# Optimization experiments

Measured on AMD Instinct MI355X. Metric: run time of the kernel, lower is better.

Reference implementation:

```python
import jax, jax.numpy as jnp
import numpy as np

B, N, D_IN, D_OUT = 2, 2048, 2048, 2048
H, G = 16, 4            # num_heads, n_kv_groups
HD = D_OUT // H         # head_dim = 128
REP = H // G            # query heads per kv head = 4


def setup_inputs() -> dict:
    key = jax.random.key(0)
    ks = jax.random.split(key, 6)
    s = lambda fan_in: 1.0 / np.sqrt(fan_in)
    return {
        "x": jax.random.normal(ks[0], (B, N, D_IN), jnp.float32),
        "Wq": jax.random.normal(ks[1], (D_IN, D_OUT), jnp.float32) * s(D_IN),
        "Wk": jax.random.normal(ks[2], (D_IN, G * HD), jnp.float32) * s(D_IN),
        "Wv": jax.random.normal(ks[3], (D_IN, G * HD), jnp.float32) * s(D_IN),
        "Wo": jax.random.normal(ks[4], (D_OUT, D_OUT), jnp.float32) * s(D_OUT),
        "bo": jnp.zeros((D_OUT,), jnp.float32),
    }


def reference(x, Wq, Wk, Wv, Wo, bo):
    b, n, _ = x.shape
    # projections
    q = (x @ Wq).reshape(b, n, G, REP, HD)   # query heads grouped: h = g*REP + r
    k = (x @ Wk).reshape(b, n, G, HD)
    v = (x @ Wv).reshape(b, n, G, HD)
    # grouped attention scores; KV broadcast over REP instead of repeat_kv
    scores = jnp.einsum('bqgrd,bkgd->bgrqk', q, k)  # [b,G,REP,N,N]
    causal = jnp.tril(jnp.ones((n, n), bool))       # allowed positions
    scores = jnp.where(causal, scores, -jnp.inf)
    w = jax.nn.softmax(scores / np.float32(np.sqrt(HD)), axis=-1)
    ctx = jnp.einsum('bgrqk,bkgd->bqgrd', w, v).reshape(b, n, D_OUT)
    return ctx @ Wo + bo
```

## Files before the change

kernel.cpp:

```cpp
#include <hip/hip_runtime.h>
#include <stdint.h>

typedef __attribute__((ext_vector_type(8))) __bf16 bf16x8;
typedef __attribute__((ext_vector_type(4))) float f32x4;
typedef __attribute__((ext_vector_type(16))) float f32x16;
typedef __attribute__((ext_vector_type(4))) short short4v;
typedef __attribute__((ext_vector_type(4))) unsigned uint4v;

static constexpr int SEQ  = 2048;
static constexpr int DQKV = 3072;
static constexpr int HD   = 128;

__device__ __forceinline__ short f2bf(float f) {
  unsigned u = __builtin_bit_cast(unsigned, f);
  u += 0x7fffu + ((u >> 16) & 1u);
  return (short)(u >> 16);
}

__device__ __forceinline__ unsigned pack2(float a, float b) {
  return (unsigned)(unsigned short)f2bf(a) | ((unsigned)(unsigned short)f2bf(b) << 16);
}

__device__ __forceinline__ void gl_lds16(const void* g, void* l) {
  __builtin_amdgcn_global_load_lds(
      (const __attribute__((address_space(1))) void*)g,
      (__attribute__((address_space(3))) void*)l, 16, 0, 0);
}

__global__ __launch_bounds__(256)
void prep_kernel(const float* __restrict__ x, const float* __restrict__ Wq,
                 const float* __restrict__ Wk, const float* __restrict__ Wv,
                 const float* __restrict__ Wo,
                 short* __restrict__ xb, short* __restrict__ WqkvT,
                 short* __restrict__ WoT) {
  int blk = blockIdx.x, tid = threadIdx.x;
  if (blk < 8192) {
    int i = blk * 256 + tid;
    float4 v = reinterpret_cast<const float4*>(x)[i];
    short4v o;
    o[0] = f2bf(v.x); o[1] = f2bf(v.y); o[2] = f2bf(v.z); o[3] = f2bf(v.w);
    *reinterpret_cast<short4v*>(xb + (size_t)i * 4) = o;
    return;
  }
  blk -= 8192;
  __shared__ float tile[32][33];
  const float* in; short* out; int C, bx, by;
  if (blk < 4096)      { in = Wq; out = WqkvT;                     C = 2048; bx = blk & 63; by = blk >> 6; }
  else if (blk < 5120) { int t = blk - 4096; in = Wk; out = WqkvT + (size_t)2048 * 2048; C = 512; bx = t & 15; by = t >> 4; }
  else if (blk < 6144) { int t = blk - 5120; in = Wv; out = WqkvT + (size_t)2560 * 2048; C = 512; bx = t & 15; by = t >> 4; }
  else                 { int t = blk - 6144; in = Wo; out = WoT;   C = 2048; bx = t & 63; by = t >> 6; }
  const int R = 2048;
  int c0 = bx * 32, r0 = by * 32, tx = tid & 31, ty = tid >> 5;
  for (int i = 0; i < 4; i++)
    tile[ty + i * 8][tx] = in[(size_t)(r0 + ty + i * 8) * C + c0 + tx];
  __syncthreads();
  for (int i = 0; i < 4; i++)
    out[(size_t)(c0 + ty + i * 8) * R + r0 + tx] = f2bf(tile[tx][ty + i * 8]);
}

__global__ __launch_bounds__(256) void transpose_v_kernel(const short* __restrict__ qkv,
                                                          short* __restrict__ vT) {
  __shared__ short tile[32][33];
  int n0 = blockIdx.x * 32, c0 = blockIdx.y * 32, b = blockIdx.z;
  int tx = threadIdx.x & 31, ty = threadIdx.x >> 5;
  for (int i = 0; i < 4; i++)
    tile[ty + i * 8][tx] = qkv[(size_t)(b * SEQ + n0 + ty + i * 8) * DQKV + 2560 + c0 + tx];
  __syncthreads();
  for (int i = 0; i < 4; i++)
    vT[(size_t)(b * 512 + c0 + ty + i * 8) * SEQ + n0 + tx] = tile[tx][ty + i * 8];
}

template <int F32OUT>
__global__ __launch_bounds__(256)
void gemm_bt_kernel(const short* __restrict__ A, const short* __restrict__ BT,
                    void* __restrict__ Cout, const float* __restrict__ bias,
                    int M, int N, int K, int qcols, float qscale) {
  __shared__ __align__(16) short As[8192];
  __shared__ __align__(16) short Bs[8192];
  const int tid = threadIdx.x, lane = tid & 63, w = tid >> 6;
  const int l15 = lane & 15, quad = lane >> 4, q8 = quad * 8;
  const int row0 = blockIdx.y * 128, col0 = blockIdx.x * 128;
  const int wm = (w >> 1) * 64, wn = (w & 1) * 64;
  f32x4 acc[4][4] = {};
  const short* ga0 = A  + (size_t)(row0 + w * 16 + (lane >> 2)) * K + (lane & 3) * 8;
  const short* gb0 = BT + (size_t)(col0 + w * 16 + (lane >> 2)) * K + (lane & 3) * 8;
  for (int kt = 0; kt < K; kt += 64) {
    for (int s = 0; s < 2; s++) {
      gl_lds16(ga0 + kt + s * 32,                  As + s * 4096 + w * 512);
      gl_lds16(ga0 + (size_t)64 * K + kt + s * 32, As + s * 4096 + 2048 + w * 512);
      gl_lds16(gb0 + kt + s * 32,                  Bs + s * 4096 + w * 512);
      gl_lds16(gb0 + (size_t)64 * K + kt + s * 32, Bs + s * 4096 + 2048 + w * 512);
    }
    __syncthreads();
    for (int s = 0; s < 2; s++) {
      bf16x8 af[4], bfr[4];
      for (int i = 0; i < 4; i++)
        af[i] = *reinterpret_cast<const bf16x8*>(As + s * 4096 + (wm + i * 16 + l15) * 32 + q8);
      for (int j = 0; j < 4; j++)
        bfr[j] = *reinterpret_cast<const bf16x8*>(Bs + s * 4096 + (wn + j * 16 + l15) * 32 + q8);
      for (int i = 0; i < 4; i++)
        for (int j = 0; j < 4; j++)
          acc[i][j] = __builtin_amdgcn_mfma_f32_16x16x32_bf16(af[i], bfr[j], acc[i][j], 0, 0, 0);
    }
    __syncthreads();
  }
  if (F32OUT) {
    float* C = (float*)Cout;
    for (int j = 0; j < 4; j++) {
      int col = col0 + wn + j * 16 + l15;
      float bv = bias[col];
      for (int i = 0; i < 4; i++)
        for (int r = 0; r < 4; r++)
          C[(size_t)(row0 + wm + i * 16 + quad * 4 + r) * N + col] = acc[i][j][r] + bv;
    }
  } else {
    short* C = (short*)Cout;
    for (int j = 0; j < 4; j++) {
      int col = col0 + wn + j * 16 + l15;
      float sc = (col < qcols) ? qscale : 1.0f;
      for (int i = 0; i < 4; i++)
        for (int r = 0; r < 4; r++)
          C[(size_t)(row0 + wm + i * 16 + quad * 4 + r) * N + col] = f2bf(acc[i][j][r] * sc);
    }
  }
}

__global__ __launch_bounds__(256, 2)
void attn_kernel(const short* __restrict__ qkv, const short* __restrict__ vT,
                 short* __restrict__ ctx) {
  __shared__ __align__(16) short Ks[2 * 8192];
  __shared__ __align__(16) float Oex[2 * 4096];
  __shared__ float lbuf[4 * 32];
  const int tid = threadIdx.x, lane = tid & 63, w = tid >> 6;
  const int l31 = lane & 31, hi = lane >> 5;
  const int qh = w & 1, kh = w >> 1;
  const int idx = blockIdx.x;
  const int p = idx >> 5, h = (idx >> 1) & 15, b = idx & 1, g = h >> 2;
  const int qtA = 31 - p, qtB = p;
  const int lenA = qtA + 1, total = lenA + qtB + 1;

  auto stageK = [&](int buf, int kt) {
    const short* gk = qkv + (size_t)(b * SEQ + kt * 64) * DQKV + 2048 + g * HD;
#pragma unroll
    for (int s = 0; s < 4; s++) {
      const int r = w * 16 + s * 4 + (lane >> 4);
      gl_lds16(gk + (size_t)r * DQKV + ((lane & 15) ^ (r & 7)) * 8,
               Ks + buf * 8192 + (w * 16 + s * 4) * 128);
    }
  };

  bf16x8 qf[8];
  f32x16 o_acc[4] = {};
  float lsum = 0.f;

  stageK(0, 0);
  for (int t = 0; t < total; t++) {
    const int seg = (t >= lenA);
    const int kt = seg ? (t - lenA) : t;
    const int qt = seg ? qtB : qtA;
    const int cur = t & 1;
    __syncthreads();

    if (t == 0 || t == lenA) {
      const short* gq = qkv + (size_t)(b * SEQ + qt * 64 + qh * 32 + l31) * DQKV + h * HD + hi * 8;
#pragma unroll
      for (int d = 0; d < 8; d++) qf[d] = *reinterpret_cast<const bf16x8*>(gq + d * 16);
    }

    bf16x8 vf[4][2];
#pragma unroll
    for (int dt = 0; dt < 4; dt++)
#pragma unroll
      for (int sub = 0; sub < 2; sub++)
        vf[dt][sub] = *reinterpret_cast<const bf16x8*>(
            vT + (size_t)(b * 512 + g * HD + dt * 32 + l31) * SEQ +
            kt * 64 + (kh * 2 + sub) * 16 + hi * 8);
    __builtin_amdgcn_sched_barrier(0);

    if (t + 1 < total) {
      const int nkt = (t + 1 >= lenA) ? (t + 1 - lenA) : (t + 1);
      stageK(cur ^ 1, nkt);
    }
    __builtin_amdgcn_sched_barrier(0);

    const short* Kb = Ks + cur * 8192;
    f32x16 sa0 = {}, sa1 = {};
    __builtin_amdgcn_s_setprio(1);
#pragma unroll
    for (int d = 0; d < 4; d++) {
      bf16x8 kf0 = *reinterpret_cast<const bf16x8*>(
          Kb + (kh * 32 + l31) * 128 + (((2 * d + hi) ^ (l31 & 7)) * 8));
      bf16x8 kf1 = *reinterpret_cast<const bf16x8*>(
          Kb + (kh * 32 + l31) * 128 + (((2 * (d + 4) + hi) ^ (l31 & 7)) * 8));
      sa0 = __builtin_amdgcn_mfma_f32_32x32x16_bf16(kf0, qf[d], sa0, 0, 0, 0);
      sa1 = __builtin_amdgcn_mfma_f32_32x32x16_bf16(kf1, qf[d + 4], sa1, 0, 0, 0);
    }
    __builtin_amdgcn_s_setprio(0);
    f32x16 sa = sa0 + sa1;

    if (kt == qt) {
      const int q = qh * 32 + l31;
#pragma unroll
      for (int r = 0; r < 16; r++)
        if (kh * 32 + (r & 3) + 8 * (r >> 2) + 4 * hi > q) sa[r] = -1e38f;
    }

    float ps[16];
#pragma unroll
    for (int r = 0; r < 16; r++) ps[r] = exp2f(sa[r]);
#pragma unroll
    for (int r = 0; r < 16; r++) lsum += ps[r];
    unsigned ub[4][2];
#pragma unroll
    for (int j = 0; j < 4; j++) {
      unsigned a0 = __builtin_bit_cast(unsigned, ps[4 * j + 0]);
      unsigned a1 = __builtin_bit_cast(unsigned, ps[4 * j + 1]);
      unsigned a2 = __builtin_bit_cast(unsigned, ps[4 * j + 2]);
      unsigned a3 = __builtin_bit_cast(unsigned, ps[4 * j + 3]);
      ub[j][0] = (a0 >> 16) | (a1 & 0xffff0000u);
      ub[j][1] = (a2 >> 16) | (a3 & 0xffff0000u);
    }
    bf16x8 pfrag[2];
#pragma unroll
    for (int sub = 0; sub < 2; sub++) {
      auto s0 = __builtin_amdgcn_permlane32_swap((int)ub[2 * sub][0], (int)ub[2 * sub + 1][0], false, false);
      auto s1 = __builtin_amdgcn_permlane32_swap((int)ub[2 * sub][1], (int)ub[2 * sub + 1][1], false, false);
      uint4v uu;
      uu[0] = (unsigned)s0[0]; uu[1] = (unsigned)s1[0];
      uu[2] = (unsigned)s0[1]; uu[3] = (unsigned)s1[1];
      pfrag[sub] = __builtin_bit_cast(bf16x8, uu);
    }

    __builtin_amdgcn_s_setprio(1);
#pragma unroll
    for (int dt = 0; dt < 4; dt++)
#pragma unroll
      for (int sub = 0; sub < 2; sub++)
        o_acc[dt] = __builtin_amdgcn_mfma_f32_32x32x16_bf16(vf[dt][sub], pfrag[sub], o_acc[dt], 0, 0, 0);
    __builtin_amdgcn_s_setprio(0);

    if (kt == qt) {
      float lp = lsum + __shfl_xor(lsum, 32, 64);
      if (lane < 32) lbuf[w * 32 + l31] = lp;
      if (w >= 2) {
        float* oex = Oex + (w - 2) * 4096;
#pragma unroll
        for (int dt = 0; dt < 4; dt++)
#pragma unroll
          for (int rq = 0; rq < 4; rq++) {
            f32x4 vv = {o_acc[dt][4 * rq + 0], o_acc[dt][4 * rq + 1],
                        o_acc[dt][4 * rq + 2], o_acc[dt][4 * rq + 3]};
            *reinterpret_cast<f32x4*>(oex + ((dt * 4 + rq) * 64 + lane) * 4) = vv;
          }
      }
      __syncthreads();
      if (w < 2) {
        const float invl = 1.f / (lp + lbuf[(w ^ 2) * 32 + l31]);
        const float* oex = Oex + w * 4096;
        const size_t row = (size_t)(b * SEQ + qt * 64 + qh * 32 + l31);
#pragma unroll
        for (int dt = 0; dt < 4; dt++)
#pragma unroll
          for (int rq = 0; rq < 4; rq++) {
            f32x4 vv = *reinterpret_cast<const f32x4*>(oex + ((dt * 4 + rq) * 64 + lane) * 4);
            float e0 = (o_acc[dt][4 * rq + 0] + vv[0]) * invl;
            float e1 = (o_acc[dt][4 * rq + 1] + vv[1]) * invl;
            float e2 = (o_acc[dt][4 * rq + 2] + vv[2]) * invl;
            float e3 = (o_acc[dt][4 * rq + 3] + vv[3]) * invl;
            uint2 dd = make_uint2(pack2(e0, e1), pack2(e2, e3));
            *reinterpret_cast<uint2*>(ctx + row * 2048 + h * HD + dt * 32 + rq * 8 + hi * 4) = dd;
          }
      }
#pragma unroll
      for (int dt = 0; dt < 4; dt++)
#pragma unroll
        for (int e = 0; e < 16; e++) o_acc[dt][e] = 0.f;
      lsum = 0.f;
    }
  }
}

extern "C" void kernel_launch(void* const* d_in, const int* in_sizes, int n_in,
                              void* d_out, int out_size, void* d_ws, size_t ws_size,
                              hipStream_t stream) {
  const float* x  = (const float*)d_in[0];
  const float* Wq = (const float*)d_in[1];
  const float* Wk = (const float*)d_in[2];
  const float* Wv = (const float*)d_in[3];
  const float* Wo = (const float*)d_in[4];
  const float* bo = (const float*)d_in[5];
  float* out = (float*)d_out;

  const float sc2 = 0.08838834764831845f * 1.4426950408889634f;

  short* xb    = (short*)d_ws;
  short* WqkvT = xb    + (size_t)4096 * 2048;
  short* WoT   = WqkvT + (size_t)3072 * 2048;
  short* qkv   = WoT   + (size_t)2048 * 2048;
  short* vT    = qkv   + (size_t)4096 * 3072;
  short* ctx   = vT    + (size_t)1024 * 2048;

  prep_kernel<<<dim3(18432), dim3(256), 0, stream>>>(x, Wq, Wk, Wv, Wo, xb, WqkvT, WoT);
  gemm_bt_kernel<0><<<dim3(24, 32), dim3(256), 0, stream>>>(xb, WqkvT, qkv, nullptr,
                                                            4096, 3072, 2048, 2048, sc2);
  transpose_v_kernel<<<dim3(64, 16, 2), dim3(256), 0, stream>>>(qkv, vT);
  attn_kernel<<<dim3(512), dim3(256), 0, stream>>>(qkv, vT, ctx);
  gemm_bt_kernel<1><<<dim3(16, 32), dim3(256), 0, stream>>>(ctx, WoT, out, bo,
                                                            4096, 2048, 2048, 0, 1.0f);
}
```

Measured before the change: 312.8 us.

## Stage V tiles into LDS via async loads alongside K, shrink Oex buffer

V fragments, which were loaded from global memory straight into registers on each iteration, are now double-buffered into LDS with swizzled global_load_lds next to K and then read from LDS just before the PV MFMAs. The prefetch of the next tile is moved to the top of the loop. The cross-wave output reduction buffer is cut to a quarter by exchanging one dt slice at a time, which adds extra __syncthreads. The aim is to hide V global latency and free LDS to keep occupancy at two blocks per CU. The cost is more barriers in the epilogue and extra LDS traffic.

```diff
diff --git a/kernel.cpp b/kernel.cpp
--- a/kernel.cpp
+++ b/kernel.cpp
@@ -129,7 +129,8 @@
 void attn_kernel(const short* __restrict__ qkv, const short* __restrict__ vT,
                  short* __restrict__ ctx) {
   __shared__ __align__(16) short Ks[2 * 8192];
-  __shared__ __align__(16) float Oex[2 * 4096];
+  __shared__ __align__(16) short Vs[2 * 8192];
+  __shared__ __align__(16) float Oex[2048];
   __shared__ float lbuf[4 * 32];
   const int tid = threadIdx.x, lane = tid & 63, w = tid >> 6;
   const int l31 = lane & 31, hi = lane >> 5;
@@ -139,7 +140,7 @@
   const int qtA = 31 - p, qtB = p;
   const int lenA = qtA + 1, total = lenA + qtB + 1;
 
-  auto stageK = [&](int buf, int kt) {
+  auto stage = [&](int buf, int kt) {
     const short* gk = qkv + (size_t)(b * SEQ + kt * 64) * DQKV + 2048 + g * HD;
 #pragma unroll
     for (int s = 0; s < 4; s++) {
@@ -147,13 +148,20 @@
       gl_lds16(gk + (size_t)r * DQKV + ((lane & 15) ^ (r & 7)) * 8,
                Ks + buf * 8192 + (w * 16 + s * 4) * 128);
     }
+    const short* gv = vT + (size_t)(b * 512 + g * HD) * SEQ + kt * 64;
+#pragma unroll
+    for (int s = 0; s < 4; s++) {
+      const int r = w * 32 + s * 8 + (lane >> 3);
+      gl_lds16(gv + (size_t)r * SEQ + ((lane & 7) ^ (r & 7)) * 8,
+               Vs + buf * 8192 + (w * 32 + s * 8) * 64);
+    }
   };
 
   bf16x8 qf[8];
   f32x16 o_acc[4] = {};
   float lsum = 0.f;
 
-  stageK(0, 0);
+  stage(0, 0);
   for (int t = 0; t < total; t++) {
     const int seg = (t >= lenA);
     const int kt = seg ? (t - lenA) : t;
@@ -161,27 +169,17 @@
     const int cur = t & 1;
     __syncthreads();
 
+    if (t + 1 < total) {
+      const int nkt = (t + 1 >= lenA) ? (t + 1 - lenA) : (t + 1);
+      stage(cur ^ 1, nkt);
+    }
+    __builtin_amdgcn_sched_barrier(0);
+
     if (t == 0 || t == lenA) {
       const short* gq = qkv + (size_t)(b * SEQ + qt * 64 + qh * 32 + l31) * DQKV + h * HD + hi * 8;
 #pragma unroll
       for (int d = 0; d < 8; d++) qf[d] = *reinterpret_cast<const bf16x8*>(gq + d * 16);
     }
-
-    bf16x8 vf[4][2];
-#pragma unroll
-    for (int dt = 0; dt < 4; dt++)
-#pragma unroll
-      for (int sub = 0; sub < 2; sub++)
-        vf[dt][sub] = *reinterpret_cast<const bf16x8*>(
-            vT + (size_t)(b * 512 + g * HD + dt * 32 + l31) * SEQ +
-            kt * 64 + (kh * 2 + sub) * 16 + hi * 8);
-    __builtin_amdgcn_sched_barrier(0);
-
-    if (t + 1 < total) {
-      const int nkt = (t + 1 >= lenA) ? (t + 1 - lenA) : (t + 1);
-      stageK(cur ^ 1, nkt);
-    }
-    __builtin_amdgcn_sched_barrier(0);
 
     const short* Kb = Ks + cur * 8192;
     f32x16 sa0 = {}, sa1 = {};
@@ -231,38 +229,43 @@
       pfrag[sub] = __builtin_bit_cast(bf16x8, uu);
     }
 
+    const short* Vb = Vs + cur * 8192;
     __builtin_amdgcn_s_setprio(1);
 #pragma unroll
-    for (int dt = 0; dt < 4; dt++)
-#pragma unroll
-      for (int sub = 0; sub < 2; sub++)
-        o_acc[dt] = __builtin_amdgcn_mfma_f32_32x32x16_bf16(vf[dt][sub], pfrag[sub], o_acc[dt], 0, 0, 0);
+    for (int dt = 0; dt < 4; dt++) {
+#pragma unroll
+      for (int sub = 0; sub < 2; sub++) {
+        const int kc = kh * 4 + sub * 2 + hi;
+        bf16x8 vf = *reinterpret_cast<const bf16x8*>(
+            Vb + (dt * 32 + l31) * 64 + ((kc ^ (l31 & 7)) * 8));
+        o_acc[dt] = __builtin_amdgcn_mfma_f32_32x32x16_bf16(vf, pfrag[sub], o_acc[dt], 0, 0, 0);
+      }
+    }
     __builtin_amdgcn_s_setprio(0);
 
     if (kt == qt) {
       float lp = lsum + __shfl_xor(lsum, 32, 64);
       if (lane < 32) lbuf[w * 32 + l31] = lp;
-      if (w >= 2) {
-        float* oex = Oex + (w - 2) * 4096;
-#pragma unroll
-        for (int dt = 0; dt < 4; dt++)
+      float invl = 0.f;
+      const size_t row = (size_t)(b * SEQ + qt * 64 + qh * 32 + l31);
+#pragma unroll
+      for (int dt = 0; dt < 4; dt++) {
+        if (w >= 2) {
+          float* oex = Oex + (w - 2) * 1024;
 #pragma unroll
           for (int rq = 0; rq < 4; rq++) {
             f32x4 vv = {o_acc[dt][4 * rq + 0], o_acc[dt][4 * rq + 1],
                         o_acc[dt][4 * rq + 2], o_acc[dt][4 * rq + 3]};
-            *reinterpret_cast<f32x4*>(oex + ((dt * 4 + rq) * 64 + lane) * 4) = vv;
+            *reinterpret_cast<f32x4*>(oex + (rq * 64 + lane) * 4) = vv;
           }
-      }
-      __syncthreads();
-      if (w < 2) {
-        const float invl = 1.f / (lp + lbuf[(w ^ 2) * 32 + l31]);
-        const float* oex = Oex + w * 4096;
-        const size_t row = (size_t)(b * SEQ + qt * 64 + qh * 32 + l31);
-#pragma unroll
-        for (int dt = 0; dt < 4; dt++)
+        }
+        __syncthreads();
+        if (w < 2) {
+          if (dt == 0) invl = 1.f / (lp + lbuf[(w ^ 2) * 32 + l31]);
+          const float* oex = Oex + w * 1024;
 #pragma unroll
           for (int rq = 0; rq < 4; rq++) {
-            f32x4 vv = *reinterpret_cast<const f32x4*>(oex + ((dt * 4 + rq) * 64 + lane) * 4);
+            f32x4 vv = *reinterpret_cast<const f32x4*>(oex + (rq * 64 + lane) * 4);
             float e0 = (o_acc[dt][4 * rq + 0] + vv[0]) * invl;
             float e1 = (o_acc[dt][4 * rq + 1] + vv[1]) * invl;
             float e2 = (o_acc[dt][4 * rq + 2] + vv[2]) * invl;
@@ -270,6 +273,8 @@
             uint2 dd = make_uint2(pack2(e0, e1), pack2(e2, e3));
             *reinterpret_cast<uint2*>(ctx + row * 2048 + h * HD + dt * 32 + rq * 8 + hi * 4) = dd;
           }
+        }
+        __syncthreads();
       }
 #pragma unroll
       for (int dt = 0; dt < 4; dt++)
```

After: 281.3 us. 1.11x faster.
